# Kernel optimization log

Hardware: AMD Instinct MI355X
Metric: run time of the kernel (lower is better)

The kernel has to match this reference:

```python
import jax, jax.numpy as jnp
import numpy as np

EPS = 1e-05
TEMP = 0.01
N_BINS = 15
N = 524288
C = 100


def setup_inputs() -> dict:
    key = jax.random.key(0)
    k1, k2 = jax.random.split(key)
    logits = jax.random.normal(k1, (N, C), dtype=jnp.float32)
    labels = jax.random.randint(k2, (N,), 0, C, dtype=jnp.int64)
    return {"logits": logits, "labels": labels}


def reference(logits, labels):
    # Faithful to torch: `predictions, confidences = torch.max(log_softmax, 1)`
    # -> predictions = max log-prob VALUES, confidences = argmax INDICES.
    logp = jax.nn.log_softmax(logits, axis=1)
    predictions = jnp.max(logp, axis=1)                      # [N] float
    confidences = jnp.argmax(logp, axis=1).astype(jnp.float32)  # [N] (indices as float)

    anchors = jnp.arange(1.0 / (2.0 * N_BINS), 1.0, 1.0 / N_BINS, dtype=jnp.float32)  # [B]

    # broadcasted -(c - a)^2 / temp, softmax over bins
    diff = -(confidences[:, None] - anchors[None, :]) ** 2 / TEMP  # [N, B]
    coeffs = jax.nn.softmax(diff, axis=1)                          # [N, B]

    sum_coeffs = jnp.sum(coeffs, axis=0)                           # [B]
    denom = jnp.maximum(sum_coeffs, EPS)

    bins_confidence = jnp.sum(confidences[:, None] * coeffs, axis=0) / denom

    accuracies = (predictions == labels.astype(predictions.dtype)).astype(jnp.float32)  # [N]
    bins_accuracy = jnp.sum(accuracies[:, None] * coeffs, axis=0) / denom

    # F.normalize(p=1): L1 normalization
    bin_weights = sum_coeffs / jnp.maximum(jnp.sum(jnp.abs(sum_coeffs)), EPS)

    ece = jnp.sqrt(jnp.dot((bins_confidence - bins_accuracy) ** 2, bin_weights))
    return ece
```

## Files before the change

### kernel.cpp

```cpp
#include <hip/hip_runtime.h>
#include <math.h>

#define NBINS 15
#define NCLS 100
#define ECE_EPS 1e-5f

#define WAIT_VM25 0x4F79
#define WAIT_VM0  0x0F70

__global__ __launch_bounds__(64) void ece_hist(const float* __restrict__ logits,
                                               const int* __restrict__ labels,
                                               int* __restrict__ g_cnt,
                                               float* __restrict__ g_acc,
                                               int n_rows) {
    __shared__ float s_rows[2][64 * NCLS];
    __shared__ int   s_cnt[NCLS];
    __shared__ float s_accs[NCLS];

    const int lane = threadIdx.x;
    #pragma unroll
    for (int i = lane; i < NCLS; i += 64) { s_cnt[i] = 0; s_accs[i] = 0.0f; }

    const int n_chunks = n_rows >> 6;
    const int rot = (lane >> 3) & 7;

    int chunk = blockIdx.x;
    if (chunk < n_chunks) {
        const float* gbase = logits + (size_t)chunk * (64 * NCLS);
        #pragma unroll
        for (int j = 0; j < 25; ++j) {
            __builtin_amdgcn_global_load_lds(
                (const __attribute__((address_space(1))) void*)(gbase + (size_t)(j * 64 + lane) * 4),
                (__attribute__((address_space(3))) void*)(&s_rows[0][j * 256]),
                16, 0, 0);
        }
    }

    int buf = 0;
    while (chunk < n_chunks) {
        const int next = chunk + gridDim.x;
        const int lab = labels[chunk * 64 + lane];
        if (next < n_chunks) {
            const float* gbase = logits + (size_t)next * (64 * NCLS);
            #pragma unroll
            for (int j = 0; j < 25; ++j) {
                __builtin_amdgcn_global_load_lds(
                    (const __attribute__((address_space(1))) void*)(gbase + (size_t)(j * 64 + lane) * 4),
                    (__attribute__((address_space(3))) void*)(&s_rows[buf ^ 1][j * 256]),
                    16, 0, 0);
            }
            __builtin_amdgcn_s_waitcnt(WAIT_VM25);
        } else {
            __builtin_amdgcn_s_waitcnt(WAIT_VM0);
        }

        const float4* __restrict__ rp = (const float4*)&s_rows[buf][lane * NCLS];

        float m = -INFINITY; int mi = 1 << 30;
        #pragma unroll
        for (int j = 0; j < 25; ++j) {
            int jj = j + rot; jj -= (jj >= 25) ? 25 : 0;
            const float4 x = rp[jj];
            const int base = 4 * jj;
            if (x.x > m || (x.x == m && base     < mi)) { m = x.x; mi = base;     }
            if (x.y > m || (x.y == m && base + 1 < mi)) { m = x.y; mi = base + 1; }
            if (x.z > m || (x.z == m && base + 2 < mi)) { m = x.z; mi = base + 2; }
            if (x.w > m || (x.w == m && base + 3 < mi)) { m = x.w; mi = base + 3; }
        }

        float s0 = 0.0f, s1 = 0.0f, s2 = 0.0f, s3 = 0.0f;
        #pragma unroll
        for (int j = 0; j < 25; ++j) {
            int jj = j + rot; jj -= (jj >= 25) ? 25 : 0;
            const float4 x = rp[jj];
            s0 += __expf(x.x - m);
            s1 += __expf(x.y - m);
            s2 += __expf(x.z - m);
            s3 += __expf(x.w - m);
        }
        const float pred = -__logf((s0 + s1) + (s2 + s3));

        atomicAdd(&s_cnt[mi], 1);
        if (pred == (float)lab) atomicAdd(&s_accs[mi], 1.0f);

        buf ^= 1;
        chunk = next;
    }

    const int tail_start = n_chunks << 6;
    if (blockIdx.x == 0 && tail_start + lane < n_rows) {
        const float* row = logits + (size_t)(tail_start + lane) * NCLS;
        float m = -INFINITY; int mi = 0;
        for (int c = 0; c < NCLS; ++c) { const float x = row[c]; if (x > m) { m = x; mi = c; } }
        float s = 0.0f;
        for (int c = 0; c < NCLS; ++c) s += __expf(row[c] - m);
        const float pred = -__logf(s);
        atomicAdd(&s_cnt[mi], 1);
        if (pred == (float)labels[tail_start + lane]) atomicAdd(&s_accs[mi], 1.0f);
    }

    #pragma unroll
    for (int i = lane; i < NCLS; i += 64) {
        if (s_cnt[i])          atomicAdd(&g_cnt[i], s_cnt[i]);
        if (s_accs[i] != 0.0f) atomicAdd(&g_acc[i], s_accs[i]);
    }
}

__global__ void ece_final(const int* __restrict__ g_cnt,
                          const float* __restrict__ g_acc,
                          float* __restrict__ out) {
    __shared__ float s_bins[3 * NBINS];
    const int tid = threadIdx.x;
    if (tid < 3 * NBINS) s_bins[tid] = 0.0f;
    __syncthreads();

    if (tid < NCLS) {
        const float cnt  = (float)g_cnt[tid];
        const float accv = g_acc[tid];
        const float conf = (float)tid;
        float diff[NBINS];
        float dm = -INFINITY;
        #pragma unroll
        for (int b = 0; b < NBINS; ++b) {
            const float a = (float)(2 * b + 1) * (1.0f / 30.0f);
            const float d = conf - a;
            diff[b] = -(d * d) * 100.0f;
            dm = fmaxf(dm, diff[b]);
        }
        float es = 0.0f;
        float e[NBINS];
        #pragma unroll
        for (int b = 0; b < NBINS; ++b) { e[b] = __expf(diff[b] - dm); es += e[b]; }
        const float inv = 1.0f / es;
        #pragma unroll
        for (int b = 0; b < NBINS; ++b) {
            const float coeff = e[b] * inv;
            atomicAdd(&s_bins[b],             cnt * coeff);
            atomicAdd(&s_bins[NBINS + b],     conf * cnt * coeff);
            atomicAdd(&s_bins[2 * NBINS + b], accv * coeff);
        }
    }
    __syncthreads();

    if (tid == 0) {
        float total = 0.0f;
        #pragma unroll
        for (int b = 0; b < NBINS; ++b) total += fabsf(s_bins[b]);
        const float invw = 1.0f / fmaxf(total, ECE_EPS);
        float ece = 0.0f;
        #pragma unroll
        for (int b = 0; b < NBINS; ++b) {
            const float sc = s_bins[b];
            const float denom = fmaxf(sc, ECE_EPS);
            const float bc = s_bins[NBINS + b] / denom;
            const float ba = s_bins[2 * NBINS + b] / denom;
            const float d  = bc - ba;
            ece += d * d * (sc * invw);
        }
        out[0] = sqrtf(ece);
    }
}

extern "C" void kernel_launch(void* const* d_in, const int* in_sizes, int n_in,
                              void* d_out, int out_size, void* d_ws, size_t ws_size,
                              hipStream_t stream) {
    const float* logits = (const float*)d_in[0];
    const int*   labels = (const int*)d_in[1];
    int*   g_cnt = (int*)d_ws;
    float* g_acc = (float*)((char*)d_ws + NCLS * sizeof(int));
    float* outp  = (float*)d_out;
    const int n_rows = in_sizes[1];

    hipMemsetAsync(d_ws, 0, NCLS * (sizeof(int) + sizeof(float)), stream);
    ece_hist<<<768, 64, 0, stream>>>(logits, labels, g_cnt, g_acc, n_rows);
    ece_final<<<1, 128, 0, stream>>>(g_cnt, g_acc, outp);
}
```

Before: 389.7 us.

## Prefetch next chunk into registers instead of direct-to-LDS double buffering

Replaces the double-buffered global_load_lds async copies with a register prefetch: each lane loads 25 float4 of the next chunk into registers while computing the current chunk, then writes them to a single LDS buffer at the top of the next iteration. This halves LDS usage per block and the grid is doubled to 1536 blocks to raise occupancy. It trades the explicit waitcnt-based async path for higher register pressure (100 VGPRs of prefetch) and an extra LDS write pass per chunk.

```diff
diff --git a/kernel.cpp b/kernel.cpp
--- a/kernel.cpp
+++ b/kernel.cpp
@@ -5,15 +5,12 @@
 #define NCLS 100
 #define ECE_EPS 1e-5f
 
-#define WAIT_VM25 0x4F79
-#define WAIT_VM0  0x0F70
-
 __global__ __launch_bounds__(64) void ece_hist(const float* __restrict__ logits,
                                                const int* __restrict__ labels,
                                                int* __restrict__ g_cnt,
                                                float* __restrict__ g_acc,
                                                int n_rows) {
-    __shared__ float s_rows[2][64 * NCLS];
+    __shared__ float s_rows[64 * NCLS];
     __shared__ int   s_cnt[NCLS];
     __shared__ float s_accs[NCLS];
 
@@ -23,38 +20,29 @@
 
     const int n_chunks = n_rows >> 6;
     const int rot = (lane >> 3) & 7;
+    float4* const sw = ((float4*)s_rows) + lane;
 
     int chunk = blockIdx.x;
+    float4 t[25];
     if (chunk < n_chunks) {
-        const float* gbase = logits + (size_t)chunk * (64 * NCLS);
+        const float4* gb = (const float4*)(logits + (size_t)chunk * (64 * NCLS));
         #pragma unroll
-        for (int j = 0; j < 25; ++j) {
-            __builtin_amdgcn_global_load_lds(
-                (const __attribute__((address_space(1))) void*)(gbase + (size_t)(j * 64 + lane) * 4),
-                (__attribute__((address_space(3))) void*)(&s_rows[0][j * 256]),
-                16, 0, 0);
-        }
+        for (int j = 0; j < 25; ++j) t[j] = gb[j * 64 + lane];
     }
 
-    int buf = 0;
     while (chunk < n_chunks) {
+        #pragma unroll
+        for (int j = 0; j < 25; ++j) sw[j * 64] = t[j];
+
+        const int lab = labels[chunk * 64 + lane];
         const int next = chunk + gridDim.x;
-        const int lab = labels[chunk * 64 + lane];
         if (next < n_chunks) {
-            const float* gbase = logits + (size_t)next * (64 * NCLS);
+            const float4* gb = (const float4*)(logits + (size_t)next * (64 * NCLS));
             #pragma unroll
-            for (int j = 0; j < 25; ++j) {
-                __builtin_amdgcn_global_load_lds(
-                    (const __attribute__((address_space(1))) void*)(gbase + (size_t)(j * 64 + lane) * 4),
-                    (__attribute__((address_space(3))) void*)(&s_rows[buf ^ 1][j * 256]),
-                    16, 0, 0);
-            }
-            __builtin_amdgcn_s_waitcnt(WAIT_VM25);
-        } else {
-            __builtin_amdgcn_s_waitcnt(WAIT_VM0);
+            for (int j = 0; j < 25; ++j) t[j] = gb[j * 64 + lane];
         }
 
-        const float4* __restrict__ rp = (const float4*)&s_rows[buf][lane * NCLS];
+        const float4* __restrict__ rp = (const float4*)&s_rows[lane * NCLS];
 
         float m = -INFINITY; int mi = 1 << 30;
         #pragma unroll
@@ -67,7 +55,6 @@
             if (x.z > m || (x.z == m && base + 2 < mi)) { m = x.z; mi = base + 2; }
             if (x.w > m || (x.w == m && base + 3 < mi)) { m = x.w; mi = base + 3; }
         }
-
         float s0 = 0.0f, s1 = 0.0f, s2 = 0.0f, s3 = 0.0f;
         #pragma unroll
         for (int j = 0; j < 25; ++j) {
@@ -83,7 +70,6 @@
         atomicAdd(&s_cnt[mi], 1);
         if (pred == (float)lab) atomicAdd(&s_accs[mi], 1.0f);
 
-        buf ^= 1;
         chunk = next;
     }
 
@@ -94,9 +80,8 @@
         for (int c = 0; c < NCLS; ++c) { const float x = row[c]; if (x > m) { m = x; mi = c; } }
         float s = 0.0f;
         for (int c = 0; c < NCLS; ++c) s += __expf(row[c] - m);
-        const float pred = -__logf(s);
+        if (-__logf(s) == (float)labels[tail_start + lane]) atomicAdd(&s_accs[mi], 1.0f);
         atomicAdd(&s_cnt[mi], 1);
-        if (pred == (float)labels[tail_start + lane]) atomicAdd(&s_accs[mi], 1.0f);
     }
 
     #pragma unroll
@@ -172,6 +157,6 @@
     const int n_rows = in_sizes[1];
 
     hipMemsetAsync(d_ws, 0, NCLS * (sizeof(int) + sizeof(float)), stream);
-    ece_hist<<<768, 64, 0, stream>>>(logits, labels, g_cnt, g_acc, n_rows);
+    ece_hist<<<1536, 64, 0, stream>>>(logits, labels, g_cnt, g_acc, n_rows);
     ece_final<<<1, 128, 0, stream>>>(g_cnt, g_acc, outp);
 }
```

New measurement: 425.1 us. +9.1%, slower.
